# Kernel optimization log

Measured on AMD Instinct MI355X. Metric: run time of the kernel, lower is better.

The kernel has to match this reference:

```python
import jax, jax.numpy as jnp
import numpy as np

N, D, E, H = 100000, 128, 1600000, 256  # nodes, feat dim, edges, backbone hidden
EPS = 1e-5
NEG_SLOPE = 0.01


def setup_inputs() -> dict:
    key = jax.random.key(0)
    ks = jax.random.split(key, 16)
    s = 0.02
    return {
        "x": jax.random.normal(ks[0], (N, D), dtype=jnp.float32),
        "edges": jax.random.randint(ks[1], (2, E), 0, N, dtype=jnp.int64),
        # merge layer: Linear(2D -> D)
        "W_merge": jax.random.normal(ks[2], (2 * D, D), dtype=jnp.float32) * s,
        "b_merge": jnp.zeros((D,), dtype=jnp.float32),
        # GRUCell(D, D): weights stored torch-style (3D, D)
        "W_ih": jax.random.normal(ks[3], (3 * D, D), dtype=jnp.float32) * s,
        "W_hh": jax.random.normal(ks[4], (3 * D, D), dtype=jnp.float32) * s,
        "b_ih": jnp.zeros((3 * D,), dtype=jnp.float32),
        "b_hh": jnp.zeros((3 * D,), dtype=jnp.float32),
        # backbone: Linear(D->256), BN(256), Linear(256->D), BN(D)
        "W1": jax.random.normal(ks[5], (D, H), dtype=jnp.float32) * s,
        "b1": jnp.zeros((H,), dtype=jnp.float32),
        "g1": jnp.ones((H,), dtype=jnp.float32),
        "be1": jnp.zeros((H,), dtype=jnp.float32),
        "W2": jax.random.normal(ks[6], (H, D), dtype=jnp.float32) * s,
        "b2": jnp.zeros((D,), dtype=jnp.float32),
        "g2": jnp.ones((D,), dtype=jnp.float32),
        "be2": jnp.zeros((D,), dtype=jnp.float32),
    }


def _batchnorm(y, g, b):
    m = jnp.mean(y, axis=0)
    v = jnp.var(y, axis=0)  # biased, as torch BN uses in normalization
    return g * (y - m) * jax.lax.rsqrt(v + EPS) + b


def _leaky_relu(y):
    return jnp.where(y >= 0, y, NEG_SLOPE * y)


def reference(x, edges, W_merge, b_merge, W_ih, W_hh, b_ih, b_hh,
              W1, b1, g1, be1, W2, b2, g2, be2):
    n = x.shape[0]
    src, dst = edges[0], edges[1]
    x_nbr = x[src]                                   # (E, D) gather
    agg_sum = jax.ops.segment_sum(x_nbr, dst, num_segments=n)
    agg_max = jax.ops.segment_max(x_nbr, dst, num_segments=n)
    agg_max = jnp.where(jnp.isneginf(agg_max), jnp.zeros_like(agg_max), agg_max)
    # merge 'cat' -> Linear(2D -> D)
    merged = jnp.concatenate([agg_sum, agg_max], axis=-1) @ W_merge + b_merge
    # GRUCell update: input=merged, hidden=x
    gi = merged @ W_ih.T + b_ih                      # (N, 3D)
    gh = x @ W_hh.T + b_hh                           # (N, 3D)
    i_r, i_z, i_n = jnp.split(gi, 3, axis=-1)
    h_r, h_z, h_n = jnp.split(gh, 3, axis=-1)
    r = jax.nn.sigmoid(i_r + h_r)
    z = jax.nn.sigmoid(i_z + h_z)
    nn_ = jnp.tanh(i_n + r * h_n)
    h = (1.0 - z) * nn_ + z * x
    # backbone
    y = _batchnorm(_leaky_relu(h @ W1 + b1), g1, be1)
    y = _batchnorm(_leaky_relu(y @ W2 + b2), g2, be2)
    return y
```

## Files before the change

kernel.cpp:

```cpp
#include <hip/hip_runtime.h>
#include <math.h>

#define DD 128
#define CAPB 2048
#define MAXNB 1600

typedef __attribute__((ext_vector_type(8))) short bf16x8;
typedef __attribute__((ext_vector_type(4))) float f32x4;

__device__ __forceinline__ unsigned short f2bf(float f) {
    unsigned u = __float_as_uint(f);
    unsigned r = u + 0x7FFF + ((u >> 16) & 1);
    return (unsigned short)(r >> 16);
}
__device__ __forceinline__ float bf2f(unsigned short h) {
    return __uint_as_float(((unsigned)h) << 16);
}

__device__ __forceinline__ void gld16(const unsigned short* g, unsigned short* l) {
    __builtin_amdgcn_global_load_lds(
        (const __attribute__((address_space(1))) void*)g,
        (__attribute__((address_space(3))) void*)l, 16, 0, 0);
}

__global__ void k_wsfail(float* __restrict__ out, float val, int n) {
    int i = blockIdx.x * 256 + threadIdx.x;
    if (i < n) out[i] = (i == 0) ? val : 0.0f;
}

__global__ void k_setup(const int* __restrict__ e32, int* __restrict__ flag,
                        float* __restrict__ sums, int* __restrict__ gCur, int NB,
                        const float* __restrict__ W1, const float* __restrict__ W2,
                        unsigned short* __restrict__ w1T, unsigned short* __restrict__ w2T,
                        const float* __restrict__ x, unsigned short* __restrict__ AGG,
                        int total_x) {
    const int bid = blockIdx.x;
    const int t = threadIdx.x;
    if (bid == 0) {
        if (t == 0) {
            int f = 1;
            for (int i = 1; i < 16; i += 2) f &= (e32[i] == 0);
            *flag = f;
        }
        for (int i = t; i < 768; i += 256) sums[i] = 0.0f;
    } else if (bid < 8) {
        int i = (bid - 1) * 256 + t;
        if (i < NB) gCur[i] = 0;
    } else if (bid < 136) {
        int i = (bid - 8) * 256 + t;
        int j = i >> 7, k = i & 127;
        w1T[j * 128 + k] = f2bf(W1[k * 256 + j]);
    } else if (bid < 264) {
        int i = (bid - 136) * 256 + t;
        int j = i >> 8, k = i & 255;
        w2T[j * 256 + k] = f2bf(W2[k * 128 + j]);
    } else {
        int idx = (bid - 264) * 256 + t;
        if (idx < total_x) {
            int i = idx >> 7, j = idx & 127;
            AGG[(size_t)i * 384 + 256 + j] = f2bf(x[idx]);
        }
    }
}

__global__ void k_fusew(const float* __restrict__ Wm, const float* __restrict__ Wih,
                        const float* __restrict__ Whh, const float* __restrict__ bm,
                        const float* __restrict__ b_ih, const float* __restrict__ b_hh,
                        unsigned short* __restrict__ BtG, float* __restrict__ biasG) {
    const int j = blockIdx.x;
    const int c = threadIdx.x;
    const int g = j >> 7, d = j & 127;
    const int pj = ((d >> 4) << 6) + (g << 4) + (d & 15);
    float acc = 0.0f;
    if (j < 384) {
        const float* wr = Wih + (size_t)j * 128;
        const float* wc = Wm + (size_t)c * 128;
        for (int m = 0; m < 128; m++) acc += wc[m] * wr[m];
    }
    BtG[(size_t)pj * 384 + c] = f2bf(acc);
    if (c < 128) {
        float v = 0.0f;
        if (j < 256) v = Whh[(size_t)j * 128 + c];
        else if (j >= 384) v = Whh[(size_t)(j - 128) * 128 + c];
        BtG[(size_t)pj * 384 + 256 + c] = f2bf(v);
    }
    if (c == 0) {
        float b;
        if (j < 256) b = b_ih[j] + b_hh[j];
        else if (j < 384) b = b_ih[j];
        else b = b_hh[j - 128];
        if (j < 384) {
            const float* wr = Wih + (size_t)j * 128;
            float dd = 0.0f;
            for (int m = 0; m < 128; m++) dd += bm[m] * wr[m];
            b += dd;
        }
        biasG[pj] = b;
    }
}

__global__ __launch_bounds__(256) void k_bin(const void* __restrict__ edges_raw,
                                             const int* __restrict__ flag,
                                             int* __restrict__ gCur,
                                             unsigned* __restrict__ binned,
                                             int E, int Nn, int NB) {
    __shared__ int cnt_[MAXNB];
    __shared__ int cur_[MAXNB];
    const int t = threadIdx.x;
    const int e0 = blockIdx.x * 4096;
    for (int i = t; i < NB; i += 256) cnt_[i] = 0;
    __syncthreads();
    const int is64 = *flag;
    for (int k = 0; k < 16; k++) {
        int e = e0 + k * 256 + t;
        if (e < E) {
            int d = is64 ? (int)((const long long*)edges_raw)[(size_t)E + e]
                         : ((const int*)edges_raw)[(size_t)E + e];
            d = min(max(d, 0), Nn - 1);
            atomicAdd(&cnt_[d >> 6], 1);
        }
    }
    __syncthreads();
    for (int i = t; i < NB; i += 256) {
        int c = cnt_[i];
        cur_[i] = (c > 0) ? atomicAdd(&gCur[i], c) : 0;
    }
    __syncthreads();
    for (int k = 0; k < 16; k++) {
        int e = e0 + k * 256 + t;
        if (e < E) {
            int s, d;
            if (is64) {
                s = (int)((const long long*)edges_raw)[e];
                d = (int)((const long long*)edges_raw)[(size_t)E + e];
            } else {
                s = ((const int*)edges_raw)[e];
                d = ((const int*)edges_raw)[(size_t)E + e];
            }
            s = min(max(s, 0), Nn - 1);
            d = min(max(d, 0), Nn - 1);
            int b = d >> 6;
            int p = atomicAdd(&cur_[b], 1);
            if (p < CAPB)
                binned[(size_t)b * CAPB + p] = (unsigned)s | ((unsigned)(d & 63) << 23);
        }
    }
}

__global__ __launch_bounds__(256) void k_bagg(const unsigned* __restrict__ binned,
                                              const int* __restrict__ gCur,
                                              const void* __restrict__ edges_raw,
                                              const int* __restrict__ flag,
                                              unsigned short* __restrict__ AGG,
                                              int E, int Nn) {
    __shared__ unsigned ent[CAPB];
    __shared__ unsigned lsrc[CAPB];
    __shared__ int deg_[64], off_[64], cur2_[64];
    __shared__ int sa[64], sb[64];
    const int t = threadIdx.x;
    const int wave = t >> 6;
    const int lane = t & 63;
    const int b = blockIdx.x;
    const int node0 = b << 6;
    const int nloc = min(64, Nn - node0);
    const int cnt = gCur[b];
    const int c2 = lane * 2;

    if (cnt <= CAPB) {
        for (int i = t; i < cnt; i += 256) ent[i] = binned[(size_t)b * CAPB + i];
        if (t < 64) deg_[t] = 0;
        __syncthreads();
        for (int i = t; i < cnt; i += 256) atomicAdd(&deg_[ent[i] >> 23], 1);
        __syncthreads();
        if (t < 64) sa[t] = deg_[t];
        __syncthreads();
        for (int off = 1; off < 64; off <<= 1) {
            if (t < 64) sb[t] = sa[t] + ((t >= off) ? sa[t - off] : 0);
            __syncthreads();
            if (t < 64) sa[t] = sb[t];
            __syncthreads();
        }
        if (t < 64) {
            off_[t] = sa[t] - deg_[t];
            cur2_[t] = off_[t];
        }
        __syncthreads();
        for (int i = t; i < cnt; i += 256) {
            unsigned e = ent[i];
            int dl = e >> 23;
            int p = atomicAdd(&cur2_[dl], 1);
            lsrc[p] = e & 0x7FFFFF;
        }
        __syncthreads();
        for (int ln = wave; ln < nloc; ln += 4) {
            const int o = off_[ln];
            const int d = deg_[ln];
            float sx = 0.f, sy = 0.f;
            float mx = -INFINITY, my = -INFINITY;
            int e = 0;
            for (; e + 1 < d; e += 2) {
                int s0 = lsrc[o + e];
                int s1 = lsrc[o + e + 1];
                unsigned v0 = *(const unsigned*)(AGG + (size_t)s0 * 384 + 256 + c2);
                unsigned v1 = *(const unsigned*)(AGG + (size_t)s1 * 384 + 256 + c2);
                float ax = bf2f((unsigned short)(v0 & 0xffff));
                float ay = bf2f((unsigned short)(v0 >> 16));
                float bx = bf2f((unsigned short)(v1 & 0xffff));
                float by = bf2f((unsigned short)(v1 >> 16));
                sx += ax + bx; sy += ay + by;
                mx = fmaxf(mx, fmaxf(ax, bx)); my = fmaxf(my, fmaxf(ay, by));
            }
            if (e < d) {
                int s0 = lsrc[o + e];
                unsigned v0 = *(const unsigned*)(AGG + (size_t)s0 * 384 + 256 + c2);
                float ax = bf2f((unsigned short)(v0 & 0xffff));
                float ay = bf2f((unsigned short)(v0 >> 16));
                sx += ax; sy += ay;
                mx = fmaxf(mx, ax); my = fmaxf(my, ay);
            }
            if (d == 0) { mx = 0.f; my = 0.f; }
            unsigned short* row = AGG + (size_t)(node0 + ln) * 384;
            *(unsigned*)(row + c2) = (unsigned)f2bf(sx) | ((unsigned)f2bf(sy) << 16);
            *(unsigned*)(row + 128 + c2) = (unsigned)f2bf(mx) | ((unsigned)f2bf(my) << 16);
        }
    } else {
        const int is64 = *flag;
        for (int ln = wave; ln < nloc; ln += 4) {
            const int node = node0 + ln;
            float sx = 0.f, sy = 0.f;
            float mx = -INFINITY, my = -INFINITY;
            int d = 0;
            for (int e = 0; e < E; e++) {
                int dd = is64 ? (int)((const long long*)edges_raw)[(size_t)E + e]
                              : ((const int*)edges_raw)[(size_t)E + e];
                dd = min(max(dd, 0), Nn - 1);
                if (dd == node) {
                    int s = is64 ? (int)((const long long*)edges_raw)[e]
                                 : ((const int*)edges_raw)[e];
                    s = min(max(s, 0), Nn - 1);
                    unsigned v0 = *(const unsigned*)(AGG + (size_t)s * 384 + 256 + c2);
                    float ax = bf2f((unsigned short)(v0 & 0xffff));
                    float ay = bf2f((unsigned short)(v0 >> 16));
                    sx += ax; sy += ay;
                    mx = fmaxf(mx, ax); my = fmaxf(my, ay);
                    d++;
                }
            }
            if (d == 0) { mx = 0.f; my = 0.f; }
            unsigned short* row = AGG + (size_t)node * 384;
            *(unsigned*)(row + c2) = (unsigned)f2bf(sx) | ((unsigned)f2bf(sy) << 16);
            *(unsigned*)(row + 128 + c2) = (unsigned)f2bf(mx) | ((unsigned)f2bf(my) << 16);
        }
    }
}

template <int AFFINE, int LEAKY, int STATS, int GRUE>
__global__ __launch_bounds__(256) void k_mgemm(
    const unsigned short* __restrict__ A, int lda,
    const unsigned short* __restrict__ Bt,
    const float* __restrict__ bias,
    const float* __restrict__ sumA, const float* __restrict__ sqA,
    const float* __restrict__ gA, const float* __restrict__ beA,
    unsigned short* __restrict__ Cb, int ldc,
    int M, int K, float* __restrict__ sumO, float* __restrict__ sqO, float invN,
    const unsigned short* __restrict__ Xb) {
    __shared__ unsigned short ABs[2][2][4096];
    __shared__ float sc1[256], sh1[256];
    __shared__ float ssum[128], ssq[128];
    unsigned short* RP = &ABs[0][0][0];

    const int t = threadIdx.x;
    const int lane = t & 63;
    const int wave = t >> 6;
    const int wr = (wave >> 1) * 64;
    const int wc = (wave & 1) * 64;
    const int quad = lane >> 4;
    const int l16 = lane & 15;
    const int sig = (l16 >> 1) & 3;

    const int ncb = gridDim.x;
    const int nwg = ncb * gridDim.y;
    {
    }
    int lin = blockIdx.y * ncb + blockIdx.x;
    const int qq = nwg >> 3, rr = nwg & 7;
    const int xcd = lin & 7, pos = lin >> 3;
    const int nl = (xcd < rr ? xcd * (qq + 1) : rr * (qq + 1) + (xcd - rr) * qq) + pos;
    const int j0 = (nl % ncb) * 128;
    const int r0 = (nl / ncb) * 128;

    if (AFFINE) {
        float m = sumA[t] * invN;
        float v = sqA[t] * invN - m * m;
        if (v < 0.f) v = 0.f;
        float rs = rsqrtf(v + 1e-5f);
        float sc = gA[t] * rs;
        sc1[t] = sc;
        sh1[t] = beA[t] - m * sc;
    }
    if (STATS && t < 128) { ssum[t] = 0.f; ssq[t] = 0.f; }
    if (AFFINE || STATS) __syncthreads();

    f32x4 acc[4][4];
#pragma unroll
    for (int i = 0; i < 4; i++)
#pragma unroll
        for (int j = 0; j < 4; j++) acc[i][j] = (f32x4){0.f, 0.f, 0.f, 0.f};

    const int rowl = lane >> 2;
    const int gsw8 = (((lane & 3) ^ ((lane >> 3) & 3))) * 8;

    const int srow = t >> 2;
    const int sg8 = (t & 3) * 8;
    const int swz8 = (((t & 3) ^ ((t >> 3) & 3))) * 8;
    float4 areg[2];

    auto stageA = [&](int buf, int k0) {
#pragma unroll
        for (int p = 0; p < 2; p++) {
            int row = (wave * 2 + p) * 16 + rowl;
            int gr = r0 + row;
            if (gr >= M) gr = M - 1;
            gld16(A + (size_t)gr * lda + k0 + gsw8,
                  &ABs[buf][0][(wave * 2 + p) * 512]);
        }
    };
    auto stageB = [&](int buf, int k0) {
#pragma unroll
        for (int p = 0; p < 2; p++) {
            int row = (wave * 2 + p) * 16 + rowl;
            gld16(Bt + (size_t)(j0 + row) * K + k0 + gsw8,
                  &ABs[buf][1][(wave * 2 + p) * 512]);
        }
    };
    auto loadA = [&](int k0) {
#pragma unroll
        for (int p = 0; p < 2; p++) {
            int gr = r0 + p * 64 + srow;
            areg[p] = make_float4(0.f, 0.f, 0.f, 0.f);
            if (gr < M) areg[p] = *(const float4*)(A + (size_t)gr * lda + k0 + sg8);
        }
    };
    auto writeA = [&](int buf, int k0) {
        union U8 { float4 f; unsigned short u[8]; } uv;
#pragma unroll
        for (int p = 0; p < 2; p++) {
            uv.f = areg[p];
#pragma unroll
            for (int q = 0; q < 8; q++) {
                float f = bf2f(uv.u[q]) * sc1[k0 + sg8 + q] + sh1[k0 + sg8 + q];
                uv.u[q] = f2bf(f);
            }
            *(float4*)&ABs[buf][0][(p * 64 + srow) * 32 + swz8] = uv.f;
        }
    };

    if (AFFINE) { loadA(0); writeA(0, 0); } else stageA(0, 0);
    stageB(0, 0);
    __syncthreads();

    int buf = 0;
    for (int k0 = 0; k0 < K; k0 += 32) {
        const int kn = k0 + 32;
        const bool hasNext = kn < K;
        if (hasNext) {
            if (AFFINE) loadA(kn); else stageA(buf ^ 1, kn);
            stageB(buf ^ 1, kn);
        }
        bf16x8 af[4], bfr[4];
#pragma unroll
        for (int i = 0; i < 4; i++) {
            af[i]  = *(bf16x8*)&ABs[buf][0][(wr + i * 16 + l16) * 32 + (quad ^ sig) * 8];
            bfr[i] = *(bf16x8*)&ABs[buf][1][(wc + i * 16 + l16) * 32 + (quad ^ sig) * 8];
        }
#pragma unroll
        for (int mt = 0; mt < 4; mt++)
#pragma unroll
            for (int nt = 0; nt < 4; nt++)
                acc[mt][nt] = __builtin_amdgcn_mfma_f32_16x16x32_bf16(
                    af[mt], bfr[nt], acc[mt][nt], 0, 0, 0);
        if (AFFINE && hasNext) writeA(buf ^ 1, kn);
        __syncthreads();
        buf ^= 1;
    }

    if (GRUE) {
        const int dimb = (j0 + wc) >> 2;
        const int dloc = (wc >> 2) + l16;
        const float bR = bias[j0 + wc + l16];
        const float bZ = bias[j0 + wc + 16 + l16];
        const float bI = bias[j0 + wc + 32 + l16];
        const float bH = bias[j0 + wc + 48 + l16];
#pragma unroll
        for (int mt = 0; mt < 4; mt++) {
#pragma unroll
            for (int reg = 0; reg < 4; reg++) {
                int rloc = wr + mt * 16 + quad * 4 + reg;
                int grow = r0 + rloc;
                float r = 1.0f / (1.0f + expf(-(acc[mt][0][reg] + bR)));
                float z = 1.0f / (1.0f + expf(-(acc[mt][1][reg] + bZ)));
                float nn = tanhf(acc[mt][2][reg] + bI + r * (acc[mt][3][reg] + bH));
                float xv = 0.f;
                if (grow < M) xv = bf2f(Xb[(size_t)grow * 384 + 256 + dimb + l16]);
                float h = (1.0f - z) * nn + z * xv;
                RP[rloc * 40 + dloc] = f2bf(h);
            }
        }
        __syncthreads();
#pragma unroll
        for (int p = 0; p < 2; p++) {
            int id = p * 256 + t;
            int rloc = id >> 2, ck = id & 3;
            int grow = r0 + rloc;
            if (grow < M)
                *(float4*)(Cb + (size_t)grow * ldc + (j0 >> 2) + ck * 8) =
                    *(const float4*)&RP[rloc * 40 + ck * 8];
        }
        return;
    }

#pragma unroll
    for (int half = 0; half < 2; half++) {
        if (wr == half * 64) {
#pragma unroll
            for (int nt = 0; nt < 4; nt++) {
                int colLoc = wc + nt * 16 + l16;
                float bv = bias[j0 + colLoc];
                float s = 0.f, q = 0.f;
#pragma unroll
                for (int mt = 0; mt < 4; mt++) {
#pragma unroll
                    for (int reg = 0; reg < 4; reg++) {
                        int rloc = mt * 16 + quad * 4 + reg;
                        float v = acc[mt][nt][reg] + bv;
                        if (LEAKY) v = (v >= 0.f) ? v : 0.01f * v;
                        if (STATS && (r0 + half * 64 + rloc) < M) { s += v; q += v * v; }
                        RP[rloc * 128 + colLoc] = f2bf(v);
                    }
                }
                if (STATS) {
                    atomicAdd(&ssum[colLoc], s);
                    atomicAdd(&ssq[colLoc], q);
                }
            }
        }
        __syncthreads();
#pragma unroll
        for (int p = 0; p < 4; p++) {
            int id = p * 256 + t;
            int rloc = id >> 4;
            int ck = id & 15;
            int grow = r0 + half * 64 + rloc;
            if (grow < M)
                *(float4*)(Cb + (size_t)grow * ldc + j0 + ck * 8) =
                    *(const float4*)&RP[rloc * 128 + ck * 8];
        }
        __syncthreads();
    }
    if (STATS && t < 128) {
        atomicAdd(&sumO[j0 + t], ssum[t]);
        atomicAdd(&sqO[j0 + t], ssq[t]);
    }
}

__global__ void k_affine2(const unsigned short* __restrict__ ypre, float* __restrict__ out,
                          const float* __restrict__ sum2, const float* __restrict__ sq2,
                          const float* __restrict__ g2, const float* __restrict__ be2,
                          int total, float invN) {
    __shared__ float sc[128], sh[128];
    int t = threadIdx.x;
    if (t < 128) {
        float m = sum2[t] * invN;
        float v = sq2[t] * invN - m * m;
        if (v < 0.f) v = 0.f;
        float rs = rsqrtf(v + 1e-5f);
        float s = g2[t] * rs;
        sc[t] = s;
        sh[t] = be2[t] - m * s;
    }
    __syncthreads();
    int idx = blockIdx.x * 256 + t;
    if (idx >= total) return;
    int c = idx & 127;
    out[idx] = bf2f(ypre[idx]) * sc[c] + sh[c];
}

extern "C" void kernel_launch(void* const* d_in, const int* in_sizes, int n_in,
                              void* d_out, int out_size, void* d_ws, size_t ws_size,
                              hipStream_t stream) {
    const float* x       = (const float*)d_in[0];
    const void*  edges   = d_in[1];
    const float* W_merge = (const float*)d_in[2];
    const float* b_merge = (const float*)d_in[3];
    const float* W_ih    = (const float*)d_in[4];
    const float* W_hh    = (const float*)d_in[5];
    const float* b_ih    = (const float*)d_in[6];
    const float* b_hh    = (const float*)d_in[7];
    const float* W1      = (const float*)d_in[8];
    const float* b1      = (const float*)d_in[9];
    const float* g1      = (const float*)d_in[10];
    const float* be1     = (const float*)d_in[11];
    const float* W2      = (const float*)d_in[12];
    const float* b2      = (const float*)d_in[13];
    const float* g2      = (const float*)d_in[14];
    const float* be2     = (const float*)d_in[15];

    const int N = in_sizes[0] / DD;
    const int E = in_sizes[1] / 2;
    float* out = (float*)d_out;

    size_t need = ((size_t)640 * N + 120000) * sizeof(float);
    if (ws_size < need) {
        k_wsfail<<<(out_size + 255) / 256, 256, 0, stream>>>(
            out, (float)(ws_size >> 20), out_size);
        return;
    }

    const int NB = (N + 63) >> 6;

    float* ws = (float*)d_ws;
    unsigned short* AGG  = (unsigned short*)ws;
    unsigned short* y1b  = (unsigned short*)ws;
    unsigned short* ypre = (unsigned short*)(ws + (size_t)128 * N);
    unsigned short* hb16 = (unsigned short*)(ws + (size_t)448 * N);

    unsigned* binned = (unsigned*)(ws + (size_t)512 * N);
    int* gCur = (int*)(binned + (size_t)NB * CAPB);

    float* wbase = (float*)(gCur + NB + 64);
    unsigned short* BtG = (unsigned short*)wbase;
    unsigned short* w1T = (unsigned short*)(wbase + 98304);
    unsigned short* w2T = (unsigned short*)(wbase + 98304 + 16384);
    float* biasG = wbase + 98304 + 32768;
    float* sums  = biasG + 512;
    float* sum1 = sums, *sq1 = sums + 256, *sum2 = sums + 512, *sq2 = sums + 640;
    int*   flag  = (int*)(sums + 768);

    const int nrb  = (N + 127) / 128;
    const int ncvt = (N * DD + 255) / 256;
    const float invN = 1.0f / (float)N;

    k_setup<<<264 + ncvt, 256, 0, stream>>>(
        (const int*)edges, flag, sums, gCur, NB, W1, W2, w1T, w2T, x, AGG, N * DD);
    k_fusew<<<512, 256, 0, stream>>>(W_merge, W_ih, W_hh, b_merge, b_ih, b_hh, BtG, biasG);
    k_bin<<<(E + 4095) / 4096, 256, 0, stream>>>(edges, flag, gCur, binned, E, N, NB);
    k_bagg<<<NB, 256, 0, stream>>>(binned, gCur, edges, flag, AGG, E, N);
    k_mgemm<0, 0, 0, 1><<<dim3(4, nrb), 256, 0, stream>>>(
        AGG, 384, BtG, biasG, nullptr, nullptr, nullptr, nullptr,
        hb16, 128, N, 384, nullptr, nullptr, invN, AGG);
    k_mgemm<0, 1, 1, 0><<<dim3(2, nrb), 256, 0, stream>>>(
        hb16, 128, w1T, b1, nullptr, nullptr, nullptr, nullptr,
        y1b, 256, N, 128, sum1, sq1, invN, nullptr);
    k_mgemm<1, 1, 1, 0><<<dim3(1, nrb), 256, 0, stream>>>(
        y1b, 256, w2T, b2, sum1, sq1, g1, be1,
        ypre, 128, N, 256, sum2, sq2, invN, nullptr);
    k_affine2<<<ncvt, 256, 0, stream>>>(ypre, out, sum2, sq2, g2, be2, N * DD, invN);
}
```

Measured before the change: 498.7 us.

## Vectorize x conversion, unroll gather by four, deepen GEMM prefetch, fast GRU activations

Several independent changes. The x-to-bf16 conversion now reads float4 and writes packed pairs, using a quarter as many threads. The neighbor gather loop is unrolled to four edges so more loads are in flight. The non-affine GEMM path gets a deeper prefetch using explicit waitcnt and barrier asm so global-to-LDS loads for k+64 overlap the MFMAs. GRU sigmoid and tanh switch to exp2/rcp intrinsics with a clamped row index instead of a branch, which trades some accuracy for fewer instructions.

```diff
diff --git a/kernel.cpp b/kernel.cpp
--- a/kernel.cpp
+++ b/kernel.cpp
@@ -15,6 +15,15 @@
 }
 __device__ __forceinline__ float bf2f(unsigned short h) {
     return __uint_as_float(((unsigned)h) << 16);
+}
+
+__device__ __forceinline__ float fsigm(float x) {
+    float e = __builtin_amdgcn_exp2f(-1.442695041f * x);
+    return __builtin_amdgcn_rcpf(1.0f + e);
+}
+__device__ __forceinline__ float ftanh(float x) {
+    float e = __builtin_amdgcn_exp2f(2.885390082f * x);
+    return 1.0f - 2.0f * __builtin_amdgcn_rcpf(1.0f + e);
 }
 
 __device__ __forceinline__ void gld16(const unsigned short* g, unsigned short* l) {
@@ -33,7 +42,7 @@
                         const float* __restrict__ W1, const float* __restrict__ W2,
                         unsigned short* __restrict__ w1T, unsigned short* __restrict__ w2T,
                         const float* __restrict__ x, unsigned short* __restrict__ AGG,
-                        int total_x) {
+                        int total_x4) {
     const int bid = blockIdx.x;
     const int t = threadIdx.x;
     if (bid == 0) {
@@ -56,9 +65,14 @@
         w2T[j * 256 + k] = f2bf(W2[k * 128 + j]);
     } else {
         int idx = (bid - 264) * 256 + t;
-        if (idx < total_x) {
-            int i = idx >> 7, j = idx & 127;
-            AGG[(size_t)i * 384 + 256 + j] = f2bf(x[idx]);
+        if (idx < total_x4) {
+            int i = idx >> 5, j4 = (idx & 31) * 4;
+            float4 v = *(const float4*)(x + (size_t)i * 128 + j4);
+            unsigned lo = (unsigned)f2bf(v.x) | ((unsigned)f2bf(v.y) << 16);
+            unsigned hi = (unsigned)f2bf(v.z) | ((unsigned)f2bf(v.w) << 16);
+            unsigned short* p = AGG + (size_t)i * 384 + 256 + j4;
+            *(unsigned*)(p) = lo;
+            *(unsigned*)(p + 2) = hi;
         }
     }
 }
@@ -198,19 +212,22 @@
             float sx = 0.f, sy = 0.f;
             float mx = -INFINITY, my = -INFINITY;
             int e = 0;
-            for (; e + 1 < d; e += 2) {
-                int s0 = lsrc[o + e];
-                int s1 = lsrc[o + e + 1];
+            for (; e + 3 < d; e += 4) {
+                int s0 = lsrc[o + e], s1 = lsrc[o + e + 1];
+                int s2 = lsrc[o + e + 2], s3 = lsrc[o + e + 3];
                 unsigned v0 = *(const unsigned*)(AGG + (size_t)s0 * 384 + 256 + c2);
                 unsigned v1 = *(const unsigned*)(AGG + (size_t)s1 * 384 + 256 + c2);
-                float ax = bf2f((unsigned short)(v0 & 0xffff));
-                float ay = bf2f((unsigned short)(v0 >> 16));
-                float bx = bf2f((unsigned short)(v1 & 0xffff));
-                float by = bf2f((unsigned short)(v1 >> 16));
-                sx += ax + bx; sy += ay + by;
-                mx = fmaxf(mx, fmaxf(ax, bx)); my = fmaxf(my, fmaxf(ay, by));
-            }
-            if (e < d) {
+                unsigned v2 = *(const unsigned*)(AGG + (size_t)s2 * 384 + 256 + c2);
+                unsigned v3 = *(const unsigned*)(AGG + (size_t)s3 * 384 + 256 + c2);
+                float a0 = bf2f((unsigned short)(v0 & 0xffff)), a1 = bf2f((unsigned short)(v0 >> 16));
+                float b0 = bf2f((unsigned short)(v1 & 0xffff)), b1 = bf2f((unsigned short)(v1 >> 16));
+                float c0 = bf2f((unsigned short)(v2 & 0xffff)), c1 = bf2f((unsigned short)(v2 >> 16));
+                float d0 = bf2f((unsigned short)(v3 & 0xffff)), d1 = bf2f((unsigned short)(v3 >> 16));
+                sx += (a0 + b0) + (c0 + d0); sy += (a1 + b1) + (c1 + d1);
+                mx = fmaxf(fmaxf(mx, fmaxf(a0, b0)), fmaxf(c0, d0));
+                my = fmaxf(fmaxf(my, fmaxf(a1, b1)), fmaxf(c1, d1));
+            }
+            for (; e < d; e++) {
                 int s0 = lsrc[o + e];
                 unsigned v0 = *(const unsigned*)(AGG + (size_t)s0 * 384 + 256 + c2);
                 float ax = bf2f((unsigned short)(v0 & 0xffff));
@@ -280,8 +297,6 @@
 
     const int ncb = gridDim.x;
     const int nwg = ncb * gridDim.y;
-    {
-    }
     int lin = blockIdx.y * ncb + blockIdx.x;
     const int qq = nwg >> 3, rr = nwg & 7;
     const int xcd = lin & 7, pos = lin >> 3;
@@ -355,33 +370,58 @@
         }
     };
 
-    if (AFFINE) { loadA(0); writeA(0, 0); } else stageA(0, 0);
-    stageB(0, 0);
-    __syncthreads();
-
-    int buf = 0;
-    for (int k0 = 0; k0 < K; k0 += 32) {
-        const int kn = k0 + 32;
-        const bool hasNext = kn < K;
-        if (hasNext) {
-            if (AFFINE) loadA(kn); else stageA(buf ^ 1, kn);
-            stageB(buf ^ 1, kn);
-        }
-        bf16x8 af[4], bfr[4];
-#pragma unroll
-        for (int i = 0; i < 4; i++) {
-            af[i]  = *(bf16x8*)&ABs[buf][0][(wr + i * 16 + l16) * 32 + (quad ^ sig) * 8];
-            bfr[i] = *(bf16x8*)&ABs[buf][1][(wc + i * 16 + l16) * 32 + (quad ^ sig) * 8];
-        }
-#pragma unroll
-        for (int mt = 0; mt < 4; mt++)
-#pragma unroll
-            for (int nt = 0; nt < 4; nt++)
-                acc[mt][nt] = __builtin_amdgcn_mfma_f32_16x16x32_bf16(
-                    af[mt], bfr[nt], acc[mt][nt], 0, 0, 0);
-        if (AFFINE && hasNext) writeA(buf ^ 1, kn);
-        __syncthreads();
-        buf ^= 1;
+    if (!AFFINE) {
+        stageA(0, 0); stageB(0, 0);
+        if (32 < K) { stageA(1, 32); stageB(1, 32); }
+        for (int k0 = 0; k0 < K; k0 += 32) {
+            const int cur = (k0 >> 5) & 1;
+            if (k0 + 32 < K)
+                asm volatile("s_waitcnt vmcnt(4)\n\ts_barrier" ::: "memory");
+            else
+                asm volatile("s_waitcnt vmcnt(0)\n\ts_barrier" ::: "memory");
+            bf16x8 af[4], bfr[4];
+#pragma unroll
+            for (int i = 0; i < 4; i++) {
+                af[i]  = *(bf16x8*)&ABs[cur][0][(wr + i * 16 + l16) * 32 + (quad ^ sig) * 8];
+                bfr[i] = *(bf16x8*)&ABs[cur][1][(wc + i * 16 + l16) * 32 + (quad ^ sig) * 8];
+            }
+            asm volatile("s_waitcnt lgkmcnt(0)\n\ts_barrier" ::: "memory");
+            if (k0 + 64 < K) { stageA(cur, k0 + 64); stageB(cur, k0 + 64); }
+#pragma unroll
+            for (int mt = 0; mt < 4; mt++)
+#pragma unroll
+                for (int nt = 0; nt < 4; nt++)
+                    acc[mt][nt] = __builtin_amdgcn_mfma_f32_16x16x32_bf16(
+                        af[mt], bfr[nt], acc[mt][nt], 0, 0, 0);
+        }
+    } else {
+        loadA(0); writeA(0, 0);
+        stageB(0, 0);
+        __syncthreads();
+        int buf = 0;
+        for (int k0 = 0; k0 < K; k0 += 32) {
+            const int kn = k0 + 32;
+            const bool hasNext = kn < K;
+            if (hasNext) {
+                loadA(kn);
+                stageB(buf ^ 1, kn);
+            }
+            bf16x8 af[4], bfr[4];
+#pragma unroll
+            for (int i = 0; i < 4; i++) {
+                af[i]  = *(bf16x8*)&ABs[buf][0][(wr + i * 16 + l16) * 32 + (quad ^ sig) * 8];
+                bfr[i] = *(bf16x8*)&ABs[buf][1][(wc + i * 16 + l16) * 32 + (quad ^ sig) * 8];
+            }
+#pragma unroll
+            for (int mt = 0; mt < 4; mt++)
+#pragma unroll
+                for (int nt = 0; nt < 4; nt++)
+                    acc[mt][nt] = __builtin_amdgcn_mfma_f32_16x16x32_bf16(
+                        af[mt], bfr[nt], acc[mt][nt], 0, 0, 0);
+            if (hasNext) writeA(buf ^ 1, kn);
+            __syncthreads();
+            buf ^= 1;
+        }
     }
 
     if (GRUE) {
@@ -397,11 +437,11 @@
             for (int reg = 0; reg < 4; reg++) {
                 int rloc = wr + mt * 16 + quad * 4 + reg;
                 int grow = r0 + rloc;
-                float r = 1.0f / (1.0f + expf(-(acc[mt][0][reg] + bR)));
-                float z = 1.0f / (1.0f + expf(-(acc[mt][1][reg] + bZ)));
-                float nn = tanhf(acc[mt][2][reg] + bI + r * (acc[mt][3][reg] + bH));
-                float xv = 0.f;
-                if (grow < M) xv = bf2f(Xb[(size_t)grow * 384 + 256 + dimb + l16]);
+                int gi = grow < M ? grow : M - 1;
+                float r = fsigm(acc[mt][0][reg] + bR);
+                float z = fsigm(acc[mt][1][reg] + bZ);
+                float nn = ftanh(acc[mt][2][reg] + bI + r * (acc[mt][3][reg] + bH));
+                float xv = bf2f(Xb[(size_t)gi * 384 + 256 + dimb + l16]);
                 float h = (1.0f - z) * nn + z * xv;
                 RP[rloc * 40 + dloc] = f2bf(h);
             }
@@ -538,10 +578,11 @@
 
     const int nrb  = (N + 127) / 128;
     const int ncvt = (N * DD + 255) / 256;
+    const int ncvt4 = (N * 32 + 255) / 256;
     const float invN = 1.0f / (float)N;
 
-    k_setup<<<264 + ncvt, 256, 0, stream>>>(
-        (const int*)edges, flag, sums, gCur, NB, W1, W2, w1T, w2T, x, AGG, N * DD);
+    k_setup<<<264 + ncvt4, 256, 0, stream>>>(
+        (const int*)edges, flag, sums, gCur, NB, W1, W2, w1T, w2T, x, AGG, N * 32);
     k_fusew<<<512, 256, 0, stream>>>(W_merge, W_ih, W_hh, b_merge, b_ih, b_hh, BtG, biasG);
     k_bin<<<(E + 4095) / 4096, 256, 0, stream>>>(edges, flag, gCur, binned, E, N, NB);
     k_bagg<<<NB, 256, 0, stream>>>(binned, gCur, edges, flag, AGG, E, N);
```

Result: faster. 459.1 us (-7.9%).
